# Optimization experiments

Hardware: AMD Instinct MI355X
Metric: run time of the kernel (lower is better)

Reference implementation:

```python
import jax, jax.numpy as jnp
import numpy as np

CH = 512
NUM_GROUPS = 32
EPS = 1e-6

def _xavier(key, shape):
    fan_in, fan_out = shape[1], shape[0]
    limit = np.sqrt(6.0 / (fan_in + fan_out))
    return jax.random.uniform(key, shape, jnp.float32, -limit, limit)

def setup_inputs() -> dict:
    key = jax.random.key(0)
    ks = jax.random.split(key, 6)
    B, C, H, W = 32, CH, 32, 32
    x = jax.random.normal(ks[0], (B, C, H, W), jnp.float32)
    # 1x1 conv weights stored as [C_out, C_in]; biases zero (per initialize())
    wq = _xavier(ks[1], (C, C)); wk = _xavier(ks[2], (C, C))
    wv = _xavier(ks[3], (C, C)); wp = _xavier(ks[4], (C, C))
    bq = jnp.zeros((C,)); bk = jnp.zeros((C,)); bv = jnp.zeros((C,)); bp = jnp.zeros((C,))
    gn_w = jnp.ones((C,)); gn_b = jnp.zeros((C,))
    return {"x": x, "gn_w": gn_w, "gn_b": gn_b,
            "wq": wq, "bq": bq, "wk": wk, "bk": bk,
            "wv": wv, "bv": bv, "wp": wp, "bp": bp}

def _group_norm(x, w, b):
    B, C, H, W = x.shape
    g = NUM_GROUPS
    xg = x.reshape(B, g, C // g, H, W)
    mean = xg.mean(axis=(2, 3, 4), keepdims=True)
    var = xg.var(axis=(2, 3, 4), keepdims=True)
    xn = ((xg - mean) * jax.lax.rsqrt(var + EPS)).reshape(B, C, H, W)
    return xn * w[None, :, None, None] + b[None, :, None, None]

def reference(x, gn_w, gn_b, wq, bq, wk, bk, wv, bv, wp, bp):
    B, C, H, W = x.shape
    h = _group_norm(x, gn_w, gn_b)
    hf = h.reshape(B, C, H * W)  # [B, C, N]
    # 1x1 convs == per-pixel linear over channels
    q = jnp.einsum('oc,bcn->bno', wq, hf) + bq  # [B, N, C]
    k = jnp.einsum('oc,bcn->bon', wk, hf) + bk[None, :, None]  # [B, C, N]
    v = jnp.einsum('oc,bcn->bno', wv, hf) + bv  # [B, N, C]
    attn = jnp.einsum('bqc,bck->bqk', q, k) * (C ** -0.5)  # [B, N, N]
    attn = jax.nn.softmax(attn, axis=-1)
    out = jnp.einsum('bqk,bkc->bqc', attn, v)  # [B, N, C]
    out = jnp.einsum('oc,bnc->bon', wp, out) + bp[None, :, None]  # [B, C, N]
    return x + out.reshape(B, C, H, W)
```

## Files before the change

kernel.cpp:

```cpp
#include <hip/hip_runtime.h>


#define C_DIM 512
#define N_PIX 1024
#define BATCH 32
#define CPG 16
#define EPS 1e-6f
#define SCALE 0.044194173824159216f
#define ESTRIDE 66

typedef unsigned short u16;
typedef __attribute__((ext_vector_type(8))) short bf16x8;
typedef __attribute__((ext_vector_type(4))) float f32x4;
typedef __attribute__((ext_vector_type(2))) float f32x2;

static __device__ __forceinline__ float bf2f(u16 u) {
    union { unsigned int i; float f; } v; v.i = ((unsigned int)u) << 16; return v.f;
}
static __device__ __forceinline__ u16 f2bf(float f) {
    union { float f; unsigned int i; } v; v.f = f;
    unsigned int r = v.i + 0x7fffu + ((v.i >> 16) & 1u);
    return (u16)(r >> 16);
}

static __device__ __forceinline__ void gl_lds16(const u16* g, u16* l) {
    __builtin_amdgcn_global_load_lds(
        (const __attribute__((address_space(1))) unsigned int*)g,
        (__attribute__((address_space(3))) unsigned int*)l,
        16, 0, 0);
}

#define BAR()   __builtin_amdgcn_s_barrier()
#define SCHED() __builtin_amdgcn_sched_barrier(0x7)

__global__ __launch_bounds__(256) void wconv_kernel(
        const float* __restrict__ wq, const float* __restrict__ wk,
        const float* __restrict__ wv, const float* __restrict__ wp,
        u16* __restrict__ out) {
    int i = blockIdx.x * 256 + threadIdx.x;
    int mat = i >> 16;
    const float* src = (mat == 0) ? wq : (mat == 1) ? wk : (mat == 2) ? wv : wp;
    float4 v = ((const float4*)src)[i & 65535];
    ushort4 o;
    o.x = f2bf(v.x); o.y = f2bf(v.y); o.z = f2bf(v.z); o.w = f2bf(v.w);
    *(ushort4*)&out[(size_t)i * 4] = o;
}

__global__ __launch_bounds__(256) void gn_kernel(
        const float* __restrict__ x, const float* __restrict__ gw,
        const float* __restrict__ gb, u16* __restrict__ h) {
    int blk = blockIdx.x;
    int b = blk >> 5, g = blk & 31;
    size_t base = ((size_t)(b * C_DIM + g * CPG)) * N_PIX;
    const float4* xv = (const float4*)(x + base);
    int tid = threadIdx.x;

    float s = 0.f, sq = 0.f;
    for (int i = tid; i < (CPG * N_PIX) / 4; i += 256) {
        float4 v = xv[i];
        s  += v.x + v.y + v.z + v.w;
        sq += v.x * v.x + v.y * v.y + v.z * v.z + v.w * v.w;
    }
    __shared__ float rs[256], rq[256];
    rs[tid] = s; rq[tid] = sq;
    __syncthreads();
    for (int off = 128; off > 0; off >>= 1) {
        if (tid < off) { rs[tid] += rs[tid + off]; rq[tid] += rq[tid + off]; }
        __syncthreads();
    }
    float mean = rs[0] * (1.0f / (CPG * N_PIX));
    float var  = rq[0] * (1.0f / (CPG * N_PIX)) - mean * mean;
    float inv  = rsqrtf(var + EPS);

    __shared__ u16 Ls[CPG * N_PIX];
    for (int i = tid; i < (CPG * N_PIX) / 4; i += 256) {
        int c_local = i >> 8;
        int c = g * CPG + c_local;
        float sc = gw[c] * inv;
        float sh = gb[c] - mean * sc;
        float4 v = xv[i];
        ushort4 o;
        o.x = f2bf(v.x * sc + sh); o.y = f2bf(v.y * sc + sh);
        o.z = f2bf(v.z * sc + sh); o.w = f2bf(v.w * sc + sh);
        *(ushort4*)&Ls[c_local * N_PIX + (i & 255) * 4] = o;
    }
    __syncthreads();
    u16* hb = h + (size_t)b * N_PIX * C_DIM + g * CPG;
    for (int n = tid; n < N_PIX; n += 256) {
        unsigned int pk[8];
#pragma unroll
        for (int j = 0; j < 8; ++j) {
            unsigned int lo = Ls[(2 * j) * N_PIX + n];
            unsigned int hi = Ls[(2 * j + 1) * N_PIX + n];
            pk[j] = lo | (hi << 16);
        }
        uint4* dst = (uint4*)(hb + (size_t)n * C_DIM);
        dst[0] = make_uint4(pk[0], pk[1], pk[2], pk[3]);
        dst[1] = make_uint4(pk[4], pk[5], pk[6], pk[7]);
    }
}


#define MM(mq, nq) do { \
    _Pragma("unroll") \
    for (int t_ = 0; t_ < 4; ++t_) { \
        _Pragma("unroll") \
        for (int n_ = 0; n_ < 2; ++n_) { \
            _Pragma("unroll") \
            for (int ks_ = 0; ks_ < 2; ++ks_) \
                acc[(mq)*4 + t_][(nq)*2 + n_] = \
                    __builtin_amdgcn_mfma_f32_16x16x32_bf16( \
                        af[t_][ks_], bf[(nq)*2 + n_][ks_], \
                        acc[(mq)*4 + t_][(nq)*2 + n_], 0, 0, 0); \
        } \
    } \
} while (0)

template <int MODE>
__global__ __launch_bounds__(512, 2) void gemm_kernel(
        const u16* __restrict__ A, const u16* __restrict__ B,
        void* __restrict__ Cv, void* __restrict__ Cv2,
        const float* __restrict__ bias, const float* __restrict__ bias2,
        const float* __restrict__ xres, int K,
        int rsA, int rsB, int rsC,
        long long bsA, long long bsB, long long bsC) {
    int bx = blockIdx.x, by = blockIdx.y, bz = blockIdx.z;
    int mat = 0, b = bz;
    if (MODE == 0) { mat = bz >> 5; b = bz & 31; }
    const u16* gA = A + (size_t)b * bsA + (size_t)by * 256 * rsA;
    const u16* gB;
    if (MODE == 0) gB = B + (size_t)mat * 262144 + (size_t)bx * 256 * rsB;
    else           gB = B + (size_t)b * bsB + (size_t)bx * 256 * rsB;
    void* out = (MODE == 0 && mat) ? Cv2 : Cv;
    const float* bi_p = (MODE == 0 && mat) ? bias2 : bias;

    __shared__ __align__(16) u16 smem[65536];

    int tid = threadIdx.x;
    int lane = tid & 63, wave = tid >> 6;
    int wm = wave >> 2, wn = wave & 3;
    int quad = lane >> 4, l15 = lane & 15, l7 = lane & 7;
    int srow = tid >> 3;
    int lg = (tid & 7) ^ (srow & 7);

    const int nk = K >> 6;
    const int nit = nk >> 1;

    auto STG = [&](int buf, int isB, int h, int kt) {
        const u16* g = isB ? gB : gA;
        int rs = isB ? rsB : rsA;
        const u16* src = g + (size_t)(h * 128 + srow) * rs + (size_t)kt * 64 + lg * 8;
        u16* dst = &smem[buf * 32768 + isB * 16384 + (h * 128 + srow) * 64 + (tid & 7) * 8];
        gl_lds16(src, dst);
        gl_lds16(src + (size_t)64 * rs, dst + 4096);
    };
    auto LDA = [&](int buf, int mq, int t, int ks) -> bf16x8 {
        return *(const bf16x8*)&smem[buf * 32768 +
            (wm * 128 + mq * 64 + t * 16 + l15) * 64 + (((ks * 4 + quad) ^ l7) << 3)];
    };
    auto LDB = [&](int buf, int nt, int ks) -> bf16x8 {
        return *(const bf16x8*)&smem[buf * 32768 + 16384 +
            (wn * 64 + nt * 16 + l15) * 64 + (((ks * 4 + quad) ^ l7) << 3)];
    };

    f32x4 acc[8][4];
#pragma unroll
    for (int mt = 0; mt < 8; ++mt)
#pragma unroll
        for (int nt = 0; nt < 4; ++nt)
            acc[mt][nt] = (f32x4){0.f, 0.f, 0.f, 0.f};
    bf16x8 af[4][2], bf[4][2];

    STG(0, 1, 0, 0); STG(0, 1, 1, 0);
    STG(0, 0, 0, 0); STG(0, 0, 1, 0);
    STG(1, 1, 0, 1); STG(1, 1, 1, 1);
    asm volatile("s_waitcnt vmcnt(4)" ::: "memory");
    SCHED(); BAR(); SCHED();

    for (int it = 0; it < nit; ++it) {
        const bool s = (it + 1 < nit);
        const int k1 = 2 * it + 1, k2 = 2 * it + 2, k3 = 2 * it + 3;

#pragma unroll
        for (int t = 0; t < 4; ++t)
#pragma unroll
            for (int ks = 0; ks < 2; ++ks) af[t][ks] = LDA(0, 0, t, ks);
#pragma unroll
        for (int n = 0; n < 2; ++n)
#pragma unroll
            for (int ks = 0; ks < 2; ++ks) bf[n][ks] = LDB(0, n, ks);
        STG(1, 0, 0, k1);
        SCHED(); BAR(); SCHED();
        __builtin_amdgcn_s_setprio(1); MM(0, 0); __builtin_amdgcn_s_setprio(0);
        SCHED(); BAR(); SCHED();

#pragma unroll
        for (int n = 2; n < 4; ++n)
#pragma unroll
            for (int ks = 0; ks < 2; ++ks) bf[n][ks] = LDB(0, n, ks);
        STG(1, 0, 1, k1);
        SCHED(); BAR(); SCHED();
        __builtin_amdgcn_s_setprio(1); MM(0, 1); __builtin_amdgcn_s_setprio(0);
        SCHED(); BAR(); SCHED();

#pragma unroll
        for (int t = 0; t < 4; ++t)
#pragma unroll
            for (int ks = 0; ks < 2; ++ks) af[t][ks] = LDA(0, 1, t, ks);
        if (s) STG(0, 1, 0, k2);
        SCHED(); BAR(); SCHED();
        __builtin_amdgcn_s_setprio(1); MM(1, 1); __builtin_amdgcn_s_setprio(0);
        SCHED(); BAR(); SCHED();

        if (s) STG(0, 1, 1, k2);
        SCHED(); BAR(); SCHED();
        __builtin_amdgcn_s_setprio(1); MM(1, 0); __builtin_amdgcn_s_setprio(0);
        if (s) asm volatile("s_waitcnt vmcnt(4)" ::: "memory");
        else   asm volatile("s_waitcnt vmcnt(0)" ::: "memory");
        SCHED(); BAR(); SCHED();

#pragma unroll
        for (int t = 0; t < 4; ++t)
#pragma unroll
            for (int ks = 0; ks < 2; ++ks) af[t][ks] = LDA(1, 0, t, ks);
#pragma unroll
        for (int n = 0; n < 2; ++n)
#pragma unroll
            for (int ks = 0; ks < 2; ++ks) bf[n][ks] = LDB(1, n, ks);
        if (s) STG(0, 0, 0, k2);
        SCHED(); BAR(); SCHED();
        __builtin_amdgcn_s_setprio(1); MM(0, 0); __builtin_amdgcn_s_setprio(0);
        SCHED(); BAR(); SCHED();

#pragma unroll
        for (int n = 2; n < 4; ++n)
#pragma unroll
            for (int ks = 0; ks < 2; ++ks) bf[n][ks] = LDB(1, n, ks);
        if (s) STG(0, 0, 1, k2);
        SCHED(); BAR(); SCHED();
        __builtin_amdgcn_s_setprio(1); MM(0, 1); __builtin_amdgcn_s_setprio(0);
        SCHED(); BAR(); SCHED();

#pragma unroll
        for (int t = 0; t < 4; ++t)
#pragma unroll
            for (int ks = 0; ks < 2; ++ks) af[t][ks] = LDA(1, 1, t, ks);
        if (s) STG(1, 1, 0, k3);
        SCHED(); BAR(); SCHED();
        __builtin_amdgcn_s_setprio(1); MM(1, 1); __builtin_amdgcn_s_setprio(0);
        SCHED(); BAR(); SCHED();

        if (s) STG(1, 1, 1, k3);
        SCHED(); BAR(); SCHED();
        __builtin_amdgcn_s_setprio(1); MM(1, 0); __builtin_amdgcn_s_setprio(0);
        if (s) asm volatile("s_waitcnt vmcnt(4)" ::: "memory");
        SCHED(); BAR(); SCHED();
    }

    float* ebw = (float*)smem + wave * (16 * ESTRIDE);
    int er = lane >> 4;
    int ec4 = (lane & 15) * 4;
    int colb = bx * 256 + wn * 64;
    int rowb = by * 256 + wm * 128;
#pragma unroll
    for (int mt = 0; mt < 8; ++mt) {
#pragma unroll
        for (int nt = 0; nt < 4; ++nt) {
            f32x4 a = acc[mt][nt];
#pragma unroll
            for (int reg = 0; reg < 4; ++reg)
                ebw[(quad * 4 + reg) * ESTRIDE + nt * 16 + l15] = a[reg];
        }
#pragma unroll
        for (int j = 0; j < 4; ++j) {
            int lr = er + 4 * j;
            f32x2 v0 = *(f32x2*)&ebw[lr * ESTRIDE + ec4];
            f32x2 v1 = *(f32x2*)&ebw[lr * ESTRIDE + ec4 + 2];
            int gr = rowb + mt * 16 + lr;
            int gc = colb + ec4;
            size_t cidx = (size_t)b * bsC + (size_t)gr * rsC + gc;
            if (MODE == 0) {
                float4 b4 = *(const float4*)&bi_p[gc];
                ushort4 st;
                st.x = f2bf(v0.x + b4.x); st.y = f2bf(v0.y + b4.y);
                st.z = f2bf(v1.x + b4.z); st.w = f2bf(v1.y + b4.w);
                *(ushort4*)&((u16*)out)[cidx] = st;
            } else if (MODE == 1) {
                float bi = bi_p[gr];
                ushort4 st;
                st.x = f2bf(v0.x + bi); st.y = f2bf(v0.y + bi);
                st.z = f2bf(v1.x + bi); st.w = f2bf(v1.y + bi);
                *(ushort4*)&((u16*)out)[cidx] = st;
            } else if (MODE == 2) {
                ushort4 st;
                st.x = f2bf(v0.x * SCALE); st.y = f2bf(v0.y * SCALE);
                st.z = f2bf(v1.x * SCALE); st.w = f2bf(v1.y * SCALE);
                *(ushort4*)&((u16*)out)[cidx] = st;
            } else if (MODE == 3) {
                ushort4 st;
                st.x = f2bf(v0.x); st.y = f2bf(v0.y);
                st.z = f2bf(v1.x); st.w = f2bf(v1.y);
                *(ushort4*)&((u16*)out)[cidx] = st;
            } else {
                float bi = bi_p[gr];
                float4 xr = *(const float4*)&xres[cidx];
                float4 st = make_float4(v0.x + bi + xr.x, v0.y + bi + xr.y,
                                        v1.x + bi + xr.z, v1.y + bi + xr.w);
                *(float4*)&((float*)out)[cidx] = st;
            }
        }
    }
}

__global__ __launch_bounds__(256) void softmax_kernel(u16* __restrict__ S) {
    size_t row = blockIdx.x;
    u16* p = S + row * N_PIX;
    int tid = threadIdx.x;
    ushort4 uv = *(ushort4*)&p[tid * 4];
    float4 v = make_float4(bf2f(uv.x), bf2f(uv.y), bf2f(uv.z), bf2f(uv.w));
    __shared__ float red[256];
    float m = fmaxf(fmaxf(v.x, v.y), fmaxf(v.z, v.w));
    red[tid] = m; __syncthreads();
    for (int off = 128; off > 0; off >>= 1) {
        if (tid < off) red[tid] = fmaxf(red[tid], red[tid + off]);
        __syncthreads();
    }
    float M = red[0];
    __syncthreads();
    float4 e;
    e.x = __expf(v.x - M); e.y = __expf(v.y - M);
    e.z = __expf(v.z - M); e.w = __expf(v.w - M);
    red[tid] = e.x + e.y + e.z + e.w; __syncthreads();
    for (int off = 128; off > 0; off >>= 1) {
        if (tid < off) red[tid] += red[tid + off];
        __syncthreads();
    }
    float inv = 1.0f / red[0];
    ushort4 st;
    st.x = f2bf(e.x * inv); st.y = f2bf(e.y * inv);
    st.z = f2bf(e.z * inv); st.w = f2bf(e.w * inv);
    *(ushort4*)&p[tid * 4] = st;
}

extern "C" void kernel_launch(void* const* d_in, const int* in_sizes, int n_in,
                              void* d_out, int out_size, void* d_ws, size_t ws_size,
                              hipStream_t stream) {
    const float* x    = (const float*)d_in[0];
    const float* gn_w = (const float*)d_in[1];
    const float* gn_b = (const float*)d_in[2];
    const float* wq   = (const float*)d_in[3];
    const float* bq   = (const float*)d_in[4];
    const float* wk   = (const float*)d_in[5];
    const float* bk   = (const float*)d_in[6];
    const float* wv   = (const float*)d_in[7];
    const float* bv   = (const float*)d_in[8];
    const float* wp   = (const float*)d_in[9];
    const float* bp   = (const float*)d_in[10];
    float* y = (float*)d_out;

    const size_t BCN = (size_t)BATCH * C_DIM * N_PIX;
    char* w = (char*)d_ws;
    u16* h  = (u16*)(w);
    u16* q  = (u16*)(w + 2 * BCN);
    u16* k  = (u16*)(w + 4 * BCN);
    u16* v  = (u16*)(w + 6 * BCN);
    u16* O  = (u16*)(w + 8 * BCN);
    u16* wb = (u16*)(w + 10 * BCN);
    u16* wvb = wb + 524288, *wpb = wb + 786432;
    u16* S = h;

    const long long BS = 524288;
    const long long SB = 1048576;

    wconv_kernel<<<1024, 256, 0, stream>>>(wq, wk, wv, wp, wb);
    gn_kernel<<<1024, 256, 0, stream>>>(x, gn_w, gn_b, h);

    gemm_kernel<0><<<dim3(2, 4, 64), 512, 0, stream>>>(
        h, wb, q, k, bq, bk, nullptr, 512, 512, 512, 512, BS, 0, BS);
    gemm_kernel<1><<<dim3(4, 2, 32), 512, 0, stream>>>(
        wvb, h, v, nullptr, bv, nullptr, nullptr, 512, 512, 512, 1024, 0, BS, BS);

    for (int b0 = 0; b0 < BATCH; b0 += 16) {
        gemm_kernel<2><<<dim3(4, 4, 16), 512, 0, stream>>>(
            q + (size_t)b0 * BS, k + (size_t)b0 * BS, S, nullptr,
            nullptr, nullptr, nullptr, 512, 512, 512, 1024, BS, BS, SB);
        softmax_kernel<<<16 * 1024, 256, 0, stream>>>(S);
        gemm_kernel<3><<<dim3(2, 4, 16), 512, 0, stream>>>(
            S, v + (size_t)b0 * BS, O + (size_t)b0 * BS, nullptr,
            nullptr, nullptr, nullptr, 1024, 1024, 1024, 512, SB, BS, BS);
    }

    gemm_kernel<4><<<dim3(4, 2, 32), 512, 0, stream>>>(
        wpb, O, y, nullptr, bp, nullptr, x, 512, 512, 512, 1024, 0, BS, BS);
}
```

Measured before the change: 418.3 us.

## Batch attention over all 32 images, remap workgroups across XCDs, write bf16 epilogue directly

Replaces the two-pass loop over half-batches with single launches of the QK^T, softmax and PV kernels that cover all 32 images. Score and output buffers are split across reused workspace regions (h, O, q, k), so the full batch fits without extra memory. Workgroup ids are remapped so that consecutive tiles are spread across the eight XCDs. The bf16 epilogue now converts in registers and stages bf16 through LDS, which allows 16-byte stores and halves LDS traffic. The cost is more complex pointer selection and reliance on buffer aliasing being safe, for example q and k being overwritten by O after S has been computed.

```diff
diff --git a/kernel.cpp b/kernel.cpp
--- a/kernel.cpp
+++ b/kernel.cpp
@@ -8,6 +8,7 @@
 #define EPS 1e-6f
 #define SCALE 0.044194173824159216f
 #define ESTRIDE 66
+#define ESTRU   72
 
 typedef unsigned short u16;
 typedef __attribute__((ext_vector_type(8))) short bf16x8;
@@ -118,21 +119,45 @@
 
 template <int MODE>
 __global__ __launch_bounds__(512, 2) void gemm_kernel(
-        const u16* __restrict__ A, const u16* __restrict__ B,
+        const u16* __restrict__ A, const u16* __restrict__ A2,
+        const u16* __restrict__ B, const u16* __restrict__ B2,
         void* __restrict__ Cv, void* __restrict__ Cv2,
         const float* __restrict__ bias, const float* __restrict__ bias2,
         const float* __restrict__ xres, int K,
         int rsA, int rsB, int rsC,
         long long bsA, long long bsB, long long bsC) {
-    int bx = blockIdx.x, by = blockIdx.y, bz = blockIdx.z;
+    int nx = gridDim.x, ny = gridDim.y;
+    int nwg = nx * ny * gridDim.z;
+    int flat = blockIdx.x + nx * (blockIdx.y + ny * blockIdx.z);
+    int t = (flat & 7) * (nwg >> 3) + (flat >> 3);
+    int bx = t % nx, by = (t / nx) % ny, bz = t / (nx * ny);
+
     int mat = 0, b = bz;
-    if (MODE == 0) { mat = bz >> 5; b = bz & 31; }
-    const u16* gA = A + (size_t)b * bsA + (size_t)by * 256 * rsA;
-    const u16* gB;
-    if (MODE == 0) gB = B + (size_t)mat * 262144 + (size_t)bx * 256 * rsB;
-    else           gB = B + (size_t)b * bsB + (size_t)bx * 256 * rsB;
-    void* out = (MODE == 0 && mat) ? Cv2 : Cv;
-    const float* bi_p = (MODE == 0 && mat) ? bias2 : bias;
+    const u16 *gA, *gB;
+    void* out = Cv;
+    const float* bi_p = bias;
+    if (MODE == 0) {
+        mat = bz & 1; b = bz >> 1;
+        gA = A + (size_t)b * bsA + (size_t)by * 256 * rsA;
+        gB = B + (size_t)mat * 262144 + (size_t)bx * 256 * rsB;
+        out = mat ? Cv2 : Cv;
+        bi_p = mat ? bias2 : bias;
+    } else if (MODE == 2) {
+        gA = A + (size_t)b * bsA + (size_t)by * 256 * rsA;
+        gB = B + (size_t)b * bsB + (size_t)bx * 256 * rsB;
+        out = (b >= 16) ? Cv2 : Cv;
+    } else if (MODE == 3) {
+        gA = ((b >= 16) ? A2 : A) + (size_t)(b & 15) * bsA + (size_t)by * 256 * rsA;
+        gB = B + (size_t)b * bsB + (size_t)bx * 256 * rsB;
+        out = (b >= 16) ? Cv2 : Cv;
+    } else if (MODE == 4) {
+        gA = A + (size_t)by * 256 * rsA;
+        gB = ((b >= 16) ? B2 : B) + (size_t)(b & 15) * bsB + (size_t)bx * 256 * rsB;
+    } else {
+        gA = A + (size_t)by * 256 * rsA;
+        gB = B + (size_t)b * bsB + (size_t)bx * 256 * rsB;
+    }
+    int cb = (MODE == 2 || MODE == 3) ? (b & 15) : b;
 
     __shared__ __align__(16) u16 smem[65536];
 
@@ -154,9 +179,9 @@
         gl_lds16(src, dst);
         gl_lds16(src + (size_t)64 * rs, dst + 4096);
     };
-    auto LDA = [&](int buf, int mq, int t, int ks) -> bf16x8 {
+    auto LDA = [&](int buf, int mq, int t_, int ks) -> bf16x8 {
         return *(const bf16x8*)&smem[buf * 32768 +
-            (wm * 128 + mq * 64 + t * 16 + l15) * 64 + (((ks * 4 + quad) ^ l7) << 3)];
+            (wm * 128 + mq * 64 + t_ * 16 + l15) * 64 + (((ks * 4 + quad) ^ l7) << 3)];
     };
     auto LDB = [&](int buf, int nt, int ks) -> bf16x8 {
         return *(const bf16x8*)&smem[buf * 32768 + 16384 +
@@ -182,9 +207,9 @@
         const int k1 = 2 * it + 1, k2 = 2 * it + 2, k3 = 2 * it + 3;
 
 #pragma unroll
-        for (int t = 0; t < 4; ++t)
-#pragma unroll
-            for (int ks = 0; ks < 2; ++ks) af[t][ks] = LDA(0, 0, t, ks);
+        for (int t_ = 0; t_ < 4; ++t_)
+#pragma unroll
+            for (int ks = 0; ks < 2; ++ks) af[t_][ks] = LDA(0, 0, t_, ks);
 #pragma unroll
         for (int n = 0; n < 2; ++n)
 #pragma unroll
@@ -204,9 +229,9 @@
         SCHED(); BAR(); SCHED();
 
 #pragma unroll
-        for (int t = 0; t < 4; ++t)
-#pragma unroll
-            for (int ks = 0; ks < 2; ++ks) af[t][ks] = LDA(0, 1, t, ks);
+        for (int t_ = 0; t_ < 4; ++t_)
+#pragma unroll
+            for (int ks = 0; ks < 2; ++ks) af[t_][ks] = LDA(0, 1, t_, ks);
         if (s) STG(0, 1, 0, k2);
         SCHED(); BAR(); SCHED();
         __builtin_amdgcn_s_setprio(1); MM(1, 1); __builtin_amdgcn_s_setprio(0);
@@ -220,9 +245,9 @@
         SCHED(); BAR(); SCHED();
 
 #pragma unroll
-        for (int t = 0; t < 4; ++t)
-#pragma unroll
-            for (int ks = 0; ks < 2; ++ks) af[t][ks] = LDA(1, 0, t, ks);
+        for (int t_ = 0; t_ < 4; ++t_)
+#pragma unroll
+            for (int ks = 0; ks < 2; ++ks) af[t_][ks] = LDA(1, 0, t_, ks);
 #pragma unroll
         for (int n = 0; n < 2; ++n)
 #pragma unroll
@@ -242,9 +267,9 @@
         SCHED(); BAR(); SCHED();
 
 #pragma unroll
-        for (int t = 0; t < 4; ++t)
-#pragma unroll
-            for (int ks = 0; ks < 2; ++ks) af[t][ks] = LDA(1, 1, t, ks);
+        for (int t_ = 0; t_ < 4; ++t_)
+#pragma unroll
+            for (int ks = 0; ks < 2; ++ks) af[t_][ks] = LDA(1, 1, t_, ks);
         if (s) STG(1, 1, 0, k3);
         SCHED(); BAR(); SCHED();
         __builtin_amdgcn_s_setprio(1); MM(1, 1); __builtin_amdgcn_s_setprio(0);
@@ -257,51 +282,30 @@
         SCHED(); BAR(); SCHED();
     }
 
-    float* ebw = (float*)smem + wave * (16 * ESTRIDE);
-    int er = lane >> 4;
-    int ec4 = (lane & 15) * 4;
     int colb = bx * 256 + wn * 64;
     int rowb = by * 256 + wm * 128;
-#pragma unroll
-    for (int mt = 0; mt < 8; ++mt) {
-#pragma unroll
-        for (int nt = 0; nt < 4; ++nt) {
-            f32x4 a = acc[mt][nt];
-#pragma unroll
-            for (int reg = 0; reg < 4; ++reg)
-                ebw[(quad * 4 + reg) * ESTRIDE + nt * 16 + l15] = a[reg];
-        }
-#pragma unroll
-        for (int j = 0; j < 4; ++j) {
-            int lr = er + 4 * j;
-            f32x2 v0 = *(f32x2*)&ebw[lr * ESTRIDE + ec4];
-            f32x2 v1 = *(f32x2*)&ebw[lr * ESTRIDE + ec4 + 2];
-            int gr = rowb + mt * 16 + lr;
-            int gc = colb + ec4;
-            size_t cidx = (size_t)b * bsC + (size_t)gr * rsC + gc;
-            if (MODE == 0) {
-                float4 b4 = *(const float4*)&bi_p[gc];
-                ushort4 st;
-                st.x = f2bf(v0.x + b4.x); st.y = f2bf(v0.y + b4.y);
-                st.z = f2bf(v1.x + b4.z); st.w = f2bf(v1.y + b4.w);
-                *(ushort4*)&((u16*)out)[cidx] = st;
-            } else if (MODE == 1) {
-                float bi = bi_p[gr];
-                ushort4 st;
-                st.x = f2bf(v0.x + bi); st.y = f2bf(v0.y + bi);
-                st.z = f2bf(v1.x + bi); st.w = f2bf(v1.y + bi);
-                *(ushort4*)&((u16*)out)[cidx] = st;
-            } else if (MODE == 2) {
-                ushort4 st;
-                st.x = f2bf(v0.x * SCALE); st.y = f2bf(v0.y * SCALE);
-                st.z = f2bf(v1.x * SCALE); st.w = f2bf(v1.y * SCALE);
-                *(ushort4*)&((u16*)out)[cidx] = st;
-            } else if (MODE == 3) {
-                ushort4 st;
-                st.x = f2bf(v0.x); st.y = f2bf(v0.y);
-                st.z = f2bf(v1.x); st.w = f2bf(v1.y);
-                *(ushort4*)&((u16*)out)[cidx] = st;
-            } else {
+
+    if (MODE == 4) {
+        float* ebw = (float*)smem + wave * (16 * ESTRIDE);
+        int er = lane >> 4;
+        int ec4 = (lane & 15) * 4;
+#pragma unroll
+        for (int mt = 0; mt < 8; ++mt) {
+#pragma unroll
+            for (int nt = 0; nt < 4; ++nt) {
+                f32x4 a = acc[mt][nt];
+#pragma unroll
+                for (int reg = 0; reg < 4; ++reg)
+                    ebw[(quad * 4 + reg) * ESTRIDE + nt * 16 + l15] = a[reg];
+            }
+#pragma unroll
+            for (int j = 0; j < 4; ++j) {
+                int lr = er + 4 * j;
+                f32x2 v0 = *(f32x2*)&ebw[lr * ESTRIDE + ec4];
+                f32x2 v1 = *(f32x2*)&ebw[lr * ESTRIDE + ec4 + 2];
+                int gr = rowb + mt * 16 + lr;
+                int gc = colb + ec4;
+                size_t cidx = (size_t)cb * bsC + (size_t)gr * rsC + gc;
                 float bi = bi_p[gr];
                 float4 xr = *(const float4*)&xres[cidx];
                 float4 st = make_float4(v0.x + bi + xr.x, v0.y + bi + xr.y,
@@ -309,12 +313,50 @@
                 *(float4*)&((float*)out)[cidx] = st;
             }
         }
-    }
-}
-
-__global__ __launch_bounds__(256) void softmax_kernel(u16* __restrict__ S) {
-    size_t row = blockIdx.x;
-    u16* p = S + row * N_PIX;
+    } else {
+        u16* ebw = (u16*)smem + wave * (16 * ESTRU);
+        int er = lane >> 3;
+        int ec = (lane & 7) * 8;
+        float bcol[4];
+        if (MODE == 0) {
+#pragma unroll
+            for (int nt = 0; nt < 4; ++nt)
+                bcol[nt] = bi_p[colb + nt * 16 + l15];
+        }
+#pragma unroll
+        for (int mt = 0; mt < 8; ++mt) {
+            float4 brow;
+            if (MODE == 1)
+                brow = *(const float4*)&bi_p[rowb + mt * 16 + quad * 4];
+#pragma unroll
+            for (int nt = 0; nt < 4; ++nt) {
+                f32x4 a = acc[mt][nt];
+#pragma unroll
+                for (int reg = 0; reg < 4; ++reg) {
+                    float fv = a[reg];
+                    if (MODE == 0) fv += bcol[nt];
+                    else if (MODE == 1) fv += ((const float*)&brow)[reg];
+                    else if (MODE == 2) fv *= SCALE;
+                    ebw[(quad * 4 + reg) * ESTRU + nt * 16 + l15] = f2bf(fv);
+                }
+            }
+#pragma unroll
+            for (int j = 0; j < 2; ++j) {
+                int lr = er + 8 * j;
+                bf16x8 vv = *(const bf16x8*)&ebw[lr * ESTRU + ec];
+                int gr = rowb + mt * 16 + lr;
+                size_t cidx = (size_t)cb * bsC + (size_t)gr * rsC + colb + ec;
+                *(bf16x8*)&((u16*)out)[cidx] = vv;
+            }
+        }
+    }
+}
+
+__global__ __launch_bounds__(256) void softmax_kernel(
+        u16* __restrict__ S0, u16* __restrict__ S1) {
+    int row = blockIdx.x;
+    u16* base = (row & 16384) ? S1 : S0;
+    u16* p = base + (size_t)(row & 16383) * N_PIX;
     int tid = threadIdx.x;
     ushort4 uv = *(ushort4*)&p[tid * 4];
     float4 v = make_float4(bf2f(uv.x), bf2f(uv.y), bf2f(uv.z), bf2f(uv.w));
@@ -364,10 +406,13 @@
     u16* q  = (u16*)(w + 2 * BCN);
     u16* k  = (u16*)(w + 4 * BCN);
     u16* v  = (u16*)(w + 6 * BCN);
-    u16* O  = (u16*)(w + 8 * BCN);
+    u16* Or = (u16*)(w + 8 * BCN);
     u16* wb = (u16*)(w + 10 * BCN);
     u16* wvb = wb + 524288, *wpb = wb + 786432;
-    u16* S = h;
+    u16* S0 = h;
+    u16* S1 = Or;
+    u16* O0 = q;
+    u16* O1 = k;
 
     const long long BS = 524288;
     const long long SB = 1048576;
@@ -376,20 +421,21 @@
     gn_kernel<<<1024, 256, 0, stream>>>(x, gn_w, gn_b, h);
 
     gemm_kernel<0><<<dim3(2, 4, 64), 512, 0, stream>>>(
-        h, wb, q, k, bq, bk, nullptr, 512, 512, 512, 512, BS, 0, BS);
+        h, nullptr, wb, nullptr, q, k, bq, bk, nullptr,
+        512, 512, 512, 512, BS, 0, BS);
     gemm_kernel<1><<<dim3(4, 2, 32), 512, 0, stream>>>(
-        wvb, h, v, nullptr, bv, nullptr, nullptr, 512, 512, 512, 1024, 0, BS, BS);
-
-    for (int b0 = 0; b0 < BATCH; b0 += 16) {
-        gemm_kernel<2><<<dim3(4, 4, 16), 512, 0, stream>>>(
-            q + (size_t)b0 * BS, k + (size_t)b0 * BS, S, nullptr,
-            nullptr, nullptr, nullptr, 512, 512, 512, 1024, BS, BS, SB);
-        softmax_kernel<<<16 * 1024, 256, 0, stream>>>(S);
-        gemm_kernel<3><<<dim3(2, 4, 16), 512, 0, stream>>>(
-            S, v + (size_t)b0 * BS, O + (size_t)b0 * BS, nullptr,
-            nullptr, nullptr, nullptr, 1024, 1024, 1024, 512, SB, BS, BS);
-    }
+        wvb, nullptr, h, nullptr, v, nullptr, bv, nullptr, nullptr,
+        512, 512, 512, 1024, 0, BS, BS);
+
+    gemm_kernel<2><<<dim3(4, 4, 32), 512, 0, stream>>>(
+        q, nullptr, k, nullptr, S0, S1, nullptr, nullptr, nullptr,
+        512, 512, 512, 1024, BS, BS, SB);
+    softmax_kernel<<<32 * 1024, 256, 0, stream>>>(S0, S1);
+    gemm_kernel<3><<<dim3(2, 4, 32), 512, 0, stream>>>(
+        S0, S1, v, nullptr, O0, O1, nullptr, nullptr, nullptr,
+        1024, 1024, 1024, 512, SB, BS, BS);
 
     gemm_kernel<4><<<dim3(4, 2, 32), 512, 0, stream>>>(
-        wpb, O, y, nullptr, bp, nullptr, x, 512, 512, 512, 1024, 0, BS, BS);
-}
+        wpb, nullptr, O0, O1, y, nullptr, bp, nullptr, x,
+        512, 512, 512, 1024, 0, BS, BS);
+}
```

Result: faster. 359.0 us (-14.2%).
